# Optimization experiments

Hardware: AMD Instinct MI355X
Metric: run time of the kernel (lower is better)

## Reference

```python
import jax, jax.numpy as jnp
import numpy as np

QLEN, MLEN, B, DM, H, D, NROLL = 512, 512, 8, 1024, 16, 64, 3
KLEN = QLEN + MLEN
SCALE = 1.0 / float(np.sqrt(D))
EPS = 1e-5


def setup_inputs() -> dict:
    key = jax.random.key(0)
    ks = jax.random.split(key, 5)
    h = jax.random.normal(ks[0], (QLEN, B, DM), jnp.float32)
    mems = jax.random.normal(ks[1], (MLEN, B, DM), jnp.float32)
    Wq = jax.random.normal(ks[2], (H * D, DM), jnp.float32) * 0.02
    Wkv = jax.random.normal(ks[3], (2 * H * D, DM), jnp.float32) * 0.02
    Wo = jax.random.normal(ks[4], (DM, H * D), jnp.float32) * 0.02
    ln_gamma = jnp.ones((DM,), jnp.float32)
    ln_beta = jnp.zeros((DM,), jnp.float32)
    # Transformer-XL causal mask over [mems ; h]: query i may attend keys j <= i + MLEN
    attn_mask = jnp.triu(jnp.ones((QLEN, KLEN), dtype=bool), k=1 + MLEN)
    return dict(h=h, mems=mems, Wq=Wq, Wkv=Wkv, Wo=Wo,
                ln_gamma=ln_gamma, ln_beta=ln_beta, attn_mask=attn_mask)


def _dpfp(x):
    # concat(relu(x), relu(-x)) then multiplicative roll expansion (n_roll copies)
    x = jnp.concatenate([jax.nn.relu(x), jax.nn.relu(-x)], axis=-1)  # [..., 2D]
    return jnp.concatenate([x * jnp.roll(x, i, axis=-1) for i in range(1, NROLL + 1)],
                           axis=-1)  # [..., 2*D*NROLL]


def reference(h, mems, Wq, Wkv, Wo, ln_gamma, ln_beta, attn_mask):
    qlen, bsz = h.shape[0], h.shape[1]
    c = jnp.concatenate([mems, h], axis=0)                      # [klen, B, DM]
    klen = c.shape[0]
    q = (h @ Wq.T).reshape(qlen, bsz, H, D)                     # [i, b, n, d]
    k, v = jnp.split(c @ Wkv.T, 2, axis=-1)
    k = k.reshape(klen, bsz, H, D)
    v = v.reshape(klen, bsz, H, D)
    qf = _dpfp(q)                                               # [i, b, n, 2*D*NROLL]
    kf = _dpfp(k)
    score = jnp.einsum('ibnd,jbnd->ijbn', qf, kf) * SCALE        # [i, j, b, n]
    score = jnp.where(attn_mask[:, :, None, None], 0.0, score)
    denom = jnp.sum(score, axis=1, keepdims=True) + EPS
    prob = score / denom
    attn_vec = jnp.einsum('ijbn,jbnd->ibnd', prob, v).reshape(qlen, bsz, H * D)
    attn_out = attn_vec @ Wo.T
    # post-LN residual (pre_lnorm=False)
    x = h + attn_out
    mu = jnp.mean(x, axis=-1, keepdims=True)
    var = jnp.var(x, axis=-1, keepdims=True)
    return (x - mu) / jnp.sqrt(var + EPS) * ln_gamma + ln_beta
```

## Files before the change

### kernel.cpp

```cpp
#include <hip/hip_runtime.h>

#define QLEN 512
#define MLEN 512
#define KLEN 1024
#define BB   8
#define DMODEL 1024
#define NH   16
#define HD   64
#define NF   384
#define ATT_SCALE 0.125f
#define EPSV 1e-5f

typedef float v4f __attribute__((ext_vector_type(4)));
typedef float f32x16 __attribute__((ext_vector_type(16)));
typedef short bf16x8 __attribute__((ext_vector_type(8)));
typedef long lx2 __attribute__((ext_vector_type(2)));
typedef unsigned int u32x4 __attribute__((ext_vector_type(4)));
typedef unsigned int u32x2 __attribute__((ext_vector_type(2)));
typedef unsigned short u16x8 __attribute__((ext_vector_type(8)));

__device__ __forceinline__ unsigned short f2bf(float f) {
    unsigned int x = __builtin_bit_cast(unsigned int, f);
    x += 0x7fffu + ((x >> 16) & 1u);
    return (unsigned short)(x >> 16);
}

__device__ __forceinline__ void gll16(const void* g, void* l) {
    __builtin_amdgcn_global_load_lds(
        (const __attribute__((address_space(1))) unsigned int*)g,
        (__attribute__((address_space(3))) unsigned int*)l, 16, 0, 0);
}


__global__ __launch_bounds__(256)
void cvt_bf16_kernel(const float* __restrict__ src, unsigned short* __restrict__ dst)
{
    int i = (blockIdx.x * 256 + threadIdx.x) * 4;
    v4f v = *(const v4f*)(src + i);
    unsigned int p0, p1;
    asm("v_cvt_pk_bf16_f32 %0, %1, %2" : "=v"(p0) : "v"(v[0]), "v"(v[1]));
    asm("v_cvt_pk_bf16_f32 %0, %1, %2" : "=v"(p1) : "v"(v[2]), "v"(v[3]));
    uint2 u; u.x = p0; u.y = p1;
    *(uint2*)(dst + i) = u;
}

__global__ __launch_bounds__(256)
void cvt_fp8_kernel(const float* __restrict__ h, const float* __restrict__ mems,
                    const float* __restrict__ Wkv, const float* __restrict__ Wq,
                    unsigned char* __restrict__ c8, unsigned char* __restrict__ wkv8,
                    unsigned char* __restrict__ wq8)
{
    int tid = blockIdx.x * 256 + threadIdx.x;
    const float* src; unsigned char* dstrow; float scale; int row, k0;
    if (tid < 1048576) {
        int base = tid * 8; row = base >> 10; k0 = base & 1023;
        src = (row < 4096) ? (mems + (size_t)row * 1024)
                           : (h + (size_t)(row - 4096) * 1024);
        dstrow = c8 + (size_t)row * 1024; scale = 1.f;
    } else if (tid < 1310720) {
        int t2 = tid - 1048576; int base = t2 * 8; row = base >> 10; k0 = base & 1023;
        src = Wkv + (size_t)row * 1024; dstrow = wkv8 + (size_t)row * 1024; scale = 32.f;
    } else {
        int t2 = tid - 1310720; int base = t2 * 8; row = base >> 10; k0 = base & 1023;
        src = Wq + (size_t)row * 1024; dstrow = wq8 + (size_t)row * 1024; scale = 32.f;
    }
    v4f a = *(const v4f*)(src + k0);
    v4f b = *(const v4f*)(src + k0 + 4);
    int v0 = __builtin_amdgcn_cvt_pk_fp8_f32(a[0]*scale, a[1]*scale, 0, false);
    v0     = __builtin_amdgcn_cvt_pk_fp8_f32(a[2]*scale, a[3]*scale, v0, true);
    int v1 = __builtin_amdgcn_cvt_pk_fp8_f32(b[0]*scale, b[1]*scale, 0, false);
    v1     = __builtin_amdgcn_cvt_pk_fp8_f32(b[2]*scale, b[3]*scale, v1, true);
    int kk = (k0 & 127) >> 5;
    int lg = (k0 & 31) >> 3;
    uint2 st; st.x = (unsigned int)v0; st.y = (unsigned int)v1;
    *(uint2*)(dstrow + (k0 & ~127) + (lg * 2 + (kk >> 1)) * 16 + (kk & 1) * 8) = st;
}

__global__ __launch_bounds__(256)
void mmfp8_kernel(const unsigned char* __restrict__ A8,
                  const unsigned char* __restrict__ B8,
                  unsigned short* __restrict__ outK,
                  unsigned short* __restrict__ outV)
{
    __shared__ unsigned char As[2][128 * 128];
    __shared__ unsigned char Bs[2][128 * 128];

    const int t  = threadIdx.x;
    const int w  = t >> 6;
    const int l  = t & 63;
    const int lj = l & 15;
    const int lg = l >> 4;
    const int m0 = blockIdx.x * 128;
    const int n0 = blockIdx.y * 128;
    const int wr = w >> 1, wc = w & 1;

    const int lrow8 = l >> 3;
    const int gsw   = (l & 7) ^ lrow8;

    v4f acc[4][4] = {};

    auto STAGE = [&](int s, int buf) {
        #pragma unroll
        for (int u = 0; u < 4; ++u) {
            int i  = w * 4 + u;
            int so = (i * 8 + lrow8) * 1024 + s * 128 + gsw * 16;
            gll16(A8 + (size_t)m0 * 1024 + so, (char*)As[buf] + i * 1024);
            gll16(B8 + (size_t)n0 * 1024 + so, (char*)Bs[buf] + i * 1024);
        }
    };

    STAGE(0, 0);
    STAGE(1, 1);
    asm volatile("s_waitcnt vmcnt(8)" ::: "memory");
    __builtin_amdgcn_s_barrier();

    for (int s = 0; s < 8; ++s) {
        const int cur = s & 1;

        lx2 a2[4][2], b2[4][2];
        #pragma unroll
        for (int m = 0; m < 4; ++m) {
            int row = wr * 64 + m * 16 + lj;
            #pragma unroll
            for (int gp = 0; gp < 2; ++gp) {
                int gr = lg * 2 + gp;
                a2[m][gp] = *(const lx2*)(As[cur] + row * 128 + ((gr ^ (row & 7)) * 16));
            }
        }
        #pragma unroll
        for (int nn = 0; nn < 4; ++nn) {
            int row = wc * 64 + nn * 16 + lj;
            #pragma unroll
            for (int gp = 0; gp < 2; ++gp) {
                int gr = lg * 2 + gp;
                b2[nn][gp] = *(const lx2*)(Bs[cur] + row * 128 + ((gr ^ (row & 7)) * 16));
            }
        }
        __builtin_amdgcn_s_setprio(1);
        #pragma unroll
        for (int kk = 0; kk < 4; ++kk) {
            #pragma unroll
            for (int m = 0; m < 4; ++m)
                #pragma unroll
                for (int nn = 0; nn < 4; ++nn)
                    acc[m][nn] = __builtin_amdgcn_mfma_f32_16x16x32_fp8_fp8(
                                     a2[m][kk >> 1][kk & 1], b2[nn][kk >> 1][kk & 1],
                                     acc[m][nn], 0, 0, 0);
        }
        __builtin_amdgcn_s_setprio(0);

        if (s == 7) break;
        __builtin_amdgcn_s_barrier();
        if (s < 6) {
            STAGE(s + 2, cur);
            asm volatile("s_waitcnt vmcnt(8)" ::: "memory");
        } else {
            asm volatile("s_waitcnt vmcnt(0)" ::: "memory");
        }
        __builtin_amdgcn_s_barrier();
    }

    #pragma unroll
    for (int m = 0; m < 4; ++m) {
        #pragma unroll
        for (int rr = 0; rr < 4; ++rr) {
            int row = m0 + wr * 64 + m * 16 + 4 * lg + rr;
            #pragma unroll
            for (int nn = 0; nn < 4; ++nn) {
                int col = n0 + wc * 64 + nn * 16 + lj;
                float v = acc[m][nn][rr] * 0.03125f;
                if (n0 < 1024) outK[(size_t)row * 1024 + col] = f2bf(v);
                else           outV[(size_t)row * 1024 + (col - 1024)] = f2bf(v);
            }
        }
    }
}

__global__ __launch_bounds__(256)
void mm128_kernel(const unsigned short* __restrict__ Abf,
                  const unsigned short* __restrict__ Bbf,
                  const float* __restrict__ hres,
                  float* __restrict__ xo)
{
    __shared__ unsigned short As[128 * 64];
    __shared__ unsigned short Bs[128 * 64];

    const int t  = threadIdx.x;
    const int w  = t >> 6;
    const int l  = t & 63;
    const int lj = l & 15;
    const int lg = l >> 4;
    const int m0 = blockIdx.x * 128;
    const int n0 = blockIdx.y * 128;
    const int wr = w >> 1, wc = w & 1;
    const int rsub = l >> 3;
    const int csw  = ((l & 7) ^ rsub) * 16;

    v4f acc[4][4] = {};

    for (int s = 0; s < 16; ++s) {
        const int k0b = s * 128;
        __syncthreads();
        #pragma unroll
        for (int u = 0; u < 4; ++u) {
            int ra = w * 32 + u * 8;
            gll16((const char*)Abf + (size_t)(m0 + ra + rsub) * 2048 + k0b + csw,
                  (char*)As + ra * 128);
            gll16((const char*)Bbf + (size_t)(n0 + ra + rsub) * 2048 + k0b + csw,
                  (char*)Bs + ra * 128);
        }
        __syncthreads();
        #pragma unroll
        for (int ks = 0; ks < 2; ++ks) {
            bf16x8 af[4], bfr[4];
            #pragma unroll
            for (int m = 0; m < 4; ++m) {
                int row = wr * 64 + m * 16 + lj;
                int c = ks * 4 + lg;
                af[m] = *(const bf16x8*)((const char*)As + row * 128 +
                                         ((c ^ (row & 7)) * 16));
            }
            #pragma unroll
            for (int nn = 0; nn < 4; ++nn) {
                int row = wc * 64 + nn * 16 + lj;
                int c = ks * 4 + lg;
                bfr[nn] = *(const bf16x8*)((const char*)Bs + row * 128 +
                                           ((c ^ (row & 7)) * 16));
            }
            #pragma unroll
            for (int m = 0; m < 4; ++m)
                #pragma unroll
                for (int nn = 0; nn < 4; ++nn)
                    acc[m][nn] = __builtin_amdgcn_mfma_f32_16x16x32_bf16(
                                     af[m], bfr[nn], acc[m][nn], 0, 0, 0);
        }
    }

    #pragma unroll
    for (int m = 0; m < 4; ++m) {
        #pragma unroll
        for (int rr = 0; rr < 4; ++rr) {
            int row = m0 + wr * 64 + m * 16 + 4 * lg + rr;
            #pragma unroll
            for (int nn = 0; nn < 4; ++nn) {
                int col = n0 + wc * 64 + nn * 16 + lj;
                xo[(size_t)row * 1024 + col] =
                    acc[m][nn][rr] + hres[(size_t)row * 1024 + col];
            }
        }
    }
}

__device__ __forceinline__ float gld(const unsigned short* gr, int idx) {
    return __builtin_bit_cast(float, ((unsigned int)gr[idx]) << 16);
}

template<int FBASE>
__device__ __forceinline__ void dpfp_half8(const unsigned short* __restrict__ gr,
                                           unsigned char* __restrict__ drow)
{
    #pragma unroll
    for (int c = 0; c < 12; ++c) {
        unsigned int w4[4];
        #pragma unroll
        for (int q4 = 0; q4 < 4; ++q4) {
            float p[4];
            #pragma unroll
            for (int e = 0; e < 4; ++e) {
                const int f  = FBASE + c * 16 + q4 * 4 + e;
                const int r  = (f >> 7) + 1;
                const int tt = f & 127;
                const int uu = (tt - r) & 127;
                p[e] = gld(gr, tt) * gld(gr, uu);
            }
            int v = __builtin_amdgcn_cvt_pk_fp8_f32(p[0], p[1], 0, false);
            v     = __builtin_amdgcn_cvt_pk_fp8_f32(p[2], p[3], v, true);
            w4[q4] = (unsigned int)v;
        }
        u32x4 st = {w4[0], w4[1], w4[2], w4[3]};
        *(u32x4*)(drow + c * 1024) = st;
    }
}

__global__ __launch_bounds__(256)
void dpfp_kernel(const unsigned short* __restrict__ qraw,
                 const unsigned short* __restrict__ kraw,
                 unsigned char* __restrict__ qf, unsigned char* __restrict__ kf)
{
    __shared__ unsigned short G[128 * 138];

    const int t   = threadIdx.x;
    const int blk = blockIdx.x;

    const unsigned short* src; unsigned char* dst; int b, hh, seq0;
    if (blk < 512) {
        int bh = blk >> 2, ig = blk & 3;
        b = bh >> 4; hh = bh & 15; seq0 = ig * 128;
        src = qraw; dst = qf + (size_t)bh * 196608;
    } else {
        int blk2 = blk - 512;
        int bh = blk2 >> 3, jg = blk2 & 7;
        b = bh >> 4; hh = bh & 15; seq0 = jg * 128;
        src = kraw; dst = kf + (size_t)bh * 393216;
    }

    #pragma unroll
    for (int p = 0; p < 4; ++p) {
        int u   = p * 256 + t;
        int row = u >> 3;
        int c0  = (u & 7) * 8;
        u32x4 x = *(const u32x4*)(src + ((size_t)(seq0 + row) * 8 + b) * 1024 +
                                  hh * 64 + c0);
        char* gbase = (char*)G + row * 276 + c0 * 2;
        #pragma unroll
        for (int k = 0; k < 4; ++k) {
            unsigned int xk = x[k];
            float x0 = __builtin_bit_cast(float, xk << 16);
            float x1 = __builtin_bit_cast(float, xk & 0xffff0000u);
            float a0 = fmaxf(x0, 0.f), a1 = fmaxf(x1, 0.f);
            float b0 = fmaxf(-x0, 0.f), b1 = fmaxf(-x1, 0.f);
            unsigned int lo, hig;
            asm("v_cvt_pk_bf16_f32 %0, %1, %2" : "=v"(lo) : "v"(a0), "v"(a1));
            asm("v_cvt_pk_bf16_f32 %0, %1, %2" : "=v"(hig) : "v"(b0), "v"(b1));
            *(unsigned int*)(gbase + k * 4)       = lo;
            *(unsigned int*)(gbase + 128 + k * 4) = hig;
        }
    }
    __syncthreads();

    const int w    = t >> 6;
    const int l    = t & 63;
    const int rowc = (w >> 1) * 64 + l;
    const int hs   = w & 1;
    const unsigned short* gr = G + rowc * 138;
    const int seq = seq0 + rowc;
    unsigned char* drow = dst + (size_t)(seq >> 6) * 24576 + (seq & 63) * 16 +
                          hs * 12288;
    if (hs == 0) dpfp_half8<0>(gr, drow);
    else         dpfp_half8<192>(gr, drow);
}

__global__ __launch_bounds__(256)
void vtrans_kernel(const unsigned short* __restrict__ vraw,
                   unsigned short* __restrict__ vt)
{
    __shared__ unsigned short S[256][72];
    const int t  = threadIdx.x;
    const int jc = blockIdx.x, hh = blockIdx.y, b = blockIdx.z;
    const unsigned short* src = vraw + (size_t)((jc * 256 + t) * 8 + b) * 1024 + hh * 64;
    #pragma unroll
    for (int c = 0; c < 8; ++c)
        *(u32x4*)&S[t][c * 8] = *(const u32x4*)(src + c * 8);
    __syncthreads();
    const int d = t >> 2, qq = t & 3;
    unsigned short* dst = vt + ((size_t)(b * NH + hh) * HD + d) * KLEN + jc * 256 + qq * 64;
    #pragma unroll
    for (int c8 = 0; c8 < 8; ++c8) {
        u16x8 o;
        #pragma unroll
        for (int e = 0; e < 8; ++e) o[e] = S[qq * 64 + c8 * 8 + e][d];
        *(u16x8*)(dst + c8 * 8) = o;
    }
}

__global__ __launch_bounds__(256, 2)
void attn_mfma_kernel(const unsigned char* __restrict__ qf,
                      const unsigned char* __restrict__ kf,
                      const unsigned short* __restrict__ vt,
                      unsigned short* __restrict__ avec)
{
    __shared__ unsigned char Ks[64 * 384];
    __shared__ unsigned short Vs[64 * 64];
    __shared__ float Ds[4][32];

    const int t  = threadIdx.x;
    const int w  = t >> 6;
    const int l  = t & 63;
    const int li = l & 31;
    const int hi = l >> 5;

    const int bid = blockIdx.x;
    const int it  = (bid >> 3) & 3;
    const int P   = ((bid >> 5) << 3) + (bid & 7);
    const int n   = P & 15;
    const int b   = P >> 4;

    const unsigned char* qpan = qf + (size_t)P * 196608;
    const unsigned char* kpan = kf + (size_t)P * 393216;
    const char* vpan = (const char*)(vt + (size_t)P * HD * KLEN);

    int voff[2];
    #pragma unroll
    for (int uu = 0; uu < 2; ++uu) {
        int s  = (w * 2 + uu) * 64 + l;
        int d  = s >> 3;
        int cl = s & 7;
        int cg = cl ^ (d & 7);
        voff[uu] = d * (KLEN * 2) + cg * 16;
    }

    long qfr[24];
    {
        const unsigned char* qb = qpan + (size_t)(it * 2 + (w >> 1)) * 24576 +
                                  ((w & 1) * 32 + li) * 16 + hi * 8;
        #pragma unroll
        for (int ks = 0; ks < 24; ++ks)
            qfr[ks] = *(const long*)(qb + ks * 1024);
    }

    f32x16 num[2] = {};
    float den_acc = 0.f;

    const int ig         = it * 128 + w * 32 + li;
    const int my_jt_end  = 2 * it + 8 + (w >> 1);
    const int jt_blk_end = 2 * it + 9;

    for (int jt = 0; jt <= jt_blk_end; ++jt) {
        __syncthreads();
        const unsigned char* ktile = kpan + (size_t)jt * 24576;
        #pragma unroll
        for (int u = 0; u < 6; ++u)
            gll16(ktile + (w * 6 + u) * 1024 + l * 16, Ks + (w * 6 + u) * 1024);
        const char* vtile = vpan + jt * 128;
        #pragma unroll
        for (int uu = 0; uu < 2; ++uu)
            gll16(vtile + voff[uu], (char*)Vs + (w * 2 + uu) * 1024);
        __syncthreads();

        if (jt > my_jt_end) continue;

        f32x16 sacc0 = {};
        f32x16 sacc1 = {};
        __builtin_amdgcn_s_setprio(1);
        #pragma unroll
        for (int ks = 0; ks < 24; ++ks) {
            long k0 = *(const long*)(Ks + ks * 1024 + li * 16 + hi * 8);
            long k1 = *(const long*)(Ks + ks * 1024 + (32 + li) * 16 + hi * 8);
            sacc0 = __builtin_amdgcn_mfma_f32_32x32x16_fp8_fp8(k0, qfr[ks], sacc0, 0, 0, 0);
            sacc1 = __builtin_amdgcn_mfma_f32_32x32x16_fp8_fp8(k1, qfr[ks], sacc1, 0, 0, 0);
        }
        __builtin_amdgcn_s_setprio(0);

        if (jt == my_jt_end) {
            const int joff = jt * 64 - MLEN + 4 * hi;
            #pragma unroll
            for (int reg = 0; reg < 16; ++reg) {
                int jr = (reg & 3) + 8 * (reg >> 2);
                if (joff + jr > ig)      sacc0[reg] = 0.f;
                if (joff + 32 + jr > ig) sacc1[reg] = 0.f;
            }
        }
        {
            float dpart = 0.f;
            #pragma unroll
            for (int reg = 0; reg < 16; ++reg) dpart += sacc0[reg] + sacc1[reg];
            den_acc += dpart + __shfl_xor(dpart, 32);
        }

        #pragma unroll
        for (int jf = 0; jf < 2; ++jf) {
            const f32x16 sc = jf ? sacc1 : sacc0;
            unsigned int c01, c23, c45, c67, c89, cab, ccd, cef;
            asm("v_cvt_pk_bf16_f32 %0, %1, %2" : "=v"(c01) : "v"(sc[0]),  "v"(sc[1]));
            asm("v_cvt_pk_bf16_f32 %0, %1, %2" : "=v"(c23) : "v"(sc[2]),  "v"(sc[3]));
            asm("v_cvt_pk_bf16_f32 %0, %1, %2" : "=v"(c45) : "v"(sc[4]),  "v"(sc[5]));
            asm("v_cvt_pk_bf16_f32 %0, %1, %2" : "=v"(c67) : "v"(sc[6]),  "v"(sc[7]));
            asm("v_cvt_pk_bf16_f32 %0, %1, %2" : "=v"(c89) : "v"(sc[8]),  "v"(sc[9]));
            asm("v_cvt_pk_bf16_f32 %0, %1, %2" : "=v"(cab) : "v"(sc[10]), "v"(sc[11]));
            asm("v_cvt_pk_bf16_f32 %0, %1, %2" : "=v"(ccd) : "v"(sc[12]), "v"(sc[13]));
            asm("v_cvt_pk_bf16_f32 %0, %1, %2" : "=v"(cef) : "v"(sc[14]), "v"(sc[15]));
            u32x2 r0 = __builtin_amdgcn_permlane32_swap(c01, c45, false, false);
            u32x2 r1 = __builtin_amdgcn_permlane32_swap(c23, c67, false, false);
            u32x2 r2 = __builtin_amdgcn_permlane32_swap(c89, ccd, false, false);
            u32x2 r3 = __builtin_amdgcn_permlane32_swap(cab, cef, false, false);
            u32x4 pw0 = {r0.x, r1.x, r0.y, r1.y};
            u32x4 pw1 = {r2.x, r3.x, r2.y, r3.y};
            bf16x8 pa0 = __builtin_bit_cast(bf16x8, pw0);
            bf16x8 pa1 = __builtin_bit_cast(bf16x8, pw1);
            __builtin_amdgcn_s_setprio(1);
            #pragma unroll
            for (int dd = 0; dd < 2; ++dd) {
                int d = dd * 32 + li;
                {
                    int cs = (jf * 4 + hi) ^ (d & 7);
                    bf16x8 vb = *(const bf16x8*)((const char*)Vs + d * 128 + cs * 16);
                    num[dd] = __builtin_amdgcn_mfma_f32_32x32x16_bf16(pa0, vb, num[dd], 0, 0, 0);
                }
                {
                    int cs = (jf * 4 + 2 + hi) ^ (d & 7);
                    bf16x8 vb = *(const bf16x8*)((const char*)Vs + d * 128 + cs * 16);
                    num[dd] = __builtin_amdgcn_mfma_f32_32x32x16_bf16(pa1, vb, num[dd], 0, 0, 0);
                }
            }
            __builtin_amdgcn_s_setprio(0);
        }
    }

    if (l < 32) Ds[w][l] = den_acc;
    #pragma unroll
    for (int reg = 0; reg < 16; ++reg) {
        int i_loc = (reg & 3) + 8 * (reg >> 2) + 4 * hi;
        float dv = Ds[w][i_loc];
        float minv = ATT_SCALE / (dv * ATT_SCALE + EPSV);
        int ig2 = it * 128 + w * 32 + i_loc;
        unsigned short* orow = avec + ((size_t)ig2 * BB + b) * DMODEL + n * HD;
        orow[li]      = f2bf(num[0][reg] * minv);
        orow[32 + li] = f2bf(num[1][reg] * minv);
    }
}

__global__ __launch_bounds__(256)
void ln_kernel(const float* __restrict__ x, const float* __restrict__ gamma,
               const float* __restrict__ beta, float* __restrict__ out)
{
    const int row = blockIdx.x;
    const int t = threadIdx.x;
    const float* xr = x + (size_t)row * DMODEL;
    v4f xv = *(const v4f*)(xr + (t << 2));
    float s1 = xv[0] + xv[1] + xv[2] + xv[3];
    float s2 = xv[0]*xv[0] + xv[1]*xv[1] + xv[2]*xv[2] + xv[3]*xv[3];
    #pragma unroll
    for (int off = 32; off > 0; off >>= 1) {
        s1 += __shfl_down(s1, off);
        s2 += __shfl_down(s2, off);
    }
    __shared__ float red[2][4];
    __shared__ float mv[2];
    const int wave = t >> 6;
    if ((t & 63) == 0) { red[0][wave] = s1; red[1][wave] = s2; }
    __syncthreads();
    if (t == 0) {
        float a = red[0][0] + red[0][1] + red[0][2] + red[0][3];
        float q = red[1][0] + red[1][1] + red[1][2] + red[1][3];
        float mu  = a * (1.f / DMODEL);
        float var = q * (1.f / DMODEL) - mu * mu;
        mv[0] = mu;
        mv[1] = rsqrtf(var + EPSV);
    }
    __syncthreads();
    float mu = mv[0], rs = mv[1];
    v4f gv = *(const v4f*)(gamma + (t << 2));
    v4f bv = *(const v4f*)(beta + (t << 2));
    v4f o;
    #pragma unroll
    for (int e = 0; e < 4; ++e) o[e] = (xv[e] - mu) * rs * gv[e] + bv[e];
    *(v4f*)(out + (size_t)row * DMODEL + (t << 2)) = o;
}

extern "C" void kernel_launch(void* const* d_in, const int* in_sizes, int n_in,
                              void* d_out, int out_size, void* d_ws, size_t ws_size,
                              hipStream_t stream)
{
    const float* h     = (const float*)d_in[0];
    const float* mems  = (const float*)d_in[1];
    const float* Wq    = (const float*)d_in[2];
    const float* Wkv   = (const float*)d_in[3];
    const float* Wo    = (const float*)d_in[4];
    const float* gamma = (const float*)d_in[5];
    const float* beta  = (const float*)d_in[6];

    char* ws = (char*)d_ws;
    unsigned char* qf    = (unsigned char*)(ws);
    unsigned char* kf    = (unsigned char*)(ws + 25165824);
    unsigned char* c8    = (unsigned char*)(ws + 75497472);
    unsigned char* wkv8  = (unsigned char*)(ws + 83886080);
    unsigned char* wq8   = (unsigned char*)(ws + 85983232);
    unsigned short* kraw = (unsigned short*)(ws + 150994944);
    unsigned short* vt   = kraw;
    unsigned short* vraw = (unsigned short*)(ws + 167772160);
    unsigned short* qraw = (unsigned short*)(ws + 184549376);
    unsigned short* avec = qraw;
    float* xws = (float*)(ws);

    unsigned short* wob = (unsigned short*)d_out;

    cvt_bf16_kernel<<<1024, 256, 0, stream>>>(Wo, wob);
    cvt_fp8_kernel<<<5632, 256, 0, stream>>>(h, mems, Wkv, Wq, c8, wkv8, wq8);
    mmfp8_kernel<<<dim3(64, 16), 256, 0, stream>>>(c8, wkv8, kraw, vraw);
    mmfp8_kernel<<<dim3(32, 8), 256, 0, stream>>>(c8 + 4194304, wq8, qraw, nullptr);
    dpfp_kernel<<<1536, 256, 0, stream>>>(qraw, kraw, qf, kf);
    vtrans_kernel<<<dim3(4, 16, 8), 256, 0, stream>>>(vraw, vt);
    attn_mfma_kernel<<<512, 256, 0, stream>>>(qf, kf, vt, avec);
    mm128_kernel<<<dim3(32, 8), 256, 0, stream>>>(avec, wob, h, xws);
    ln_kernel<<<4096, 256, 0, stream>>>(xws, gamma, beta, (float*)d_out);
}
```

Baseline: 172.7 us.

## Merge prologue kernels into fewer launches and drop fp8 GEMM double buffering

Folds the Wo bf16 conversion into the fp8 conversion kernel. The KV and Q fp8 GEMMs now run as one launch with a grouped tile ordering. The V transpose moves into the dpfp feature kernel, and vt gets its own workspace region so it no longer aliases kraw. The intent is to cut launch overhead and tail gaps between small kernels. In exchange, the GEMM loses its two-stage LDS double buffering and uses a plain single buffer with two syncthreads per k-step, which exposes load latency but halves LDS use.

```diff
diff --git a/kernel.cpp b/kernel.cpp
--- a/kernel.cpp
+++ b/kernel.cpp
@@ -33,24 +33,24 @@
 
 
 __global__ __launch_bounds__(256)
-void cvt_bf16_kernel(const float* __restrict__ src, unsigned short* __restrict__ dst)
-{
-    int i = (blockIdx.x * 256 + threadIdx.x) * 4;
-    v4f v = *(const v4f*)(src + i);
-    unsigned int p0, p1;
-    asm("v_cvt_pk_bf16_f32 %0, %1, %2" : "=v"(p0) : "v"(v[0]), "v"(v[1]));
-    asm("v_cvt_pk_bf16_f32 %0, %1, %2" : "=v"(p1) : "v"(v[2]), "v"(v[3]));
-    uint2 u; u.x = p0; u.y = p1;
-    *(uint2*)(dst + i) = u;
-}
-
-__global__ __launch_bounds__(256)
-void cvt_fp8_kernel(const float* __restrict__ h, const float* __restrict__ mems,
-                    const float* __restrict__ Wkv, const float* __restrict__ Wq,
-                    unsigned char* __restrict__ c8, unsigned char* __restrict__ wkv8,
-                    unsigned char* __restrict__ wq8)
-{
-    int tid = blockIdx.x * 256 + threadIdx.x;
+void cvt_kernel(const float* __restrict__ h, const float* __restrict__ mems,
+                const float* __restrict__ Wkv, const float* __restrict__ Wq,
+                const float* __restrict__ Wo,
+                unsigned char* __restrict__ c8, unsigned char* __restrict__ wkv8,
+                unsigned char* __restrict__ wq8, unsigned short* __restrict__ wob)
+{
+    int blk = blockIdx.x;
+    if (blk >= 5632) {
+        int i = ((blk - 5632) * 256 + threadIdx.x) * 4;
+        v4f v = *(const v4f*)(Wo + i);
+        unsigned int p0, p1;
+        asm("v_cvt_pk_bf16_f32 %0, %1, %2" : "=v"(p0) : "v"(v[0]), "v"(v[1]));
+        asm("v_cvt_pk_bf16_f32 %0, %1, %2" : "=v"(p1) : "v"(v[2]), "v"(v[3]));
+        uint2 u; u.x = p0; u.y = p1;
+        *(uint2*)(wob + i) = u;
+        return;
+    }
+    int tid = blk * 256 + threadIdx.x;
     const float* src; unsigned char* dstrow; float scale; int row, k0;
     if (tid < 1048576) {
         int base = tid * 8; row = base >> 10; k0 = base & 1023;
@@ -77,21 +77,38 @@
 }
 
 __global__ __launch_bounds__(256)
-void mmfp8_kernel(const unsigned char* __restrict__ A8,
-                  const unsigned char* __restrict__ B8,
-                  unsigned short* __restrict__ outK,
-                  unsigned short* __restrict__ outV)
-{
-    __shared__ unsigned char As[2][128 * 128];
-    __shared__ unsigned char Bs[2][128 * 128];
+void mmfp8_kernel(const unsigned char* __restrict__ c8,
+                  const unsigned char* __restrict__ wkv8,
+                  const unsigned char* __restrict__ wq8,
+                  unsigned short* __restrict__ kraw,
+                  unsigned short* __restrict__ vraw,
+                  unsigned short* __restrict__ qraw)
+{
+    __shared__ unsigned char As[128 * 128];
+    __shared__ unsigned char Bs[128 * 128];
+
+    const int bid = blockIdx.x;
+    const unsigned char *A8, *B8;
+    unsigned short *outK, *outV;
+    int m0, n0;
+    if (bid < 1024) {
+        int o = bid & 7, j = bid >> 3;
+        m0 = (o * 8 + (j & 7)) * 128;
+        n0 = (j >> 3) * 128;
+        A8 = c8; B8 = wkv8; outK = kraw; outV = vraw;
+    } else {
+        int d2 = bid - 1024;
+        int o = d2 & 7, j = d2 >> 3;
+        m0 = (o * 4 + (j & 3)) * 128;
+        n0 = (j >> 2) * 128;
+        A8 = c8 + 4194304; B8 = wq8; outK = qraw; outV = nullptr;
+    }
 
     const int t  = threadIdx.x;
     const int w  = t >> 6;
     const int l  = t & 63;
     const int lj = l & 15;
     const int lg = l >> 4;
-    const int m0 = blockIdx.x * 128;
-    const int n0 = blockIdx.y * 128;
     const int wr = w >> 1, wc = w & 1;
 
     const int lrow8 = l >> 3;
@@ -99,23 +116,16 @@
 
     v4f acc[4][4] = {};
 
-    auto STAGE = [&](int s, int buf) {
+    for (int s = 0; s < 8; ++s) {
+        __syncthreads();
         #pragma unroll
         for (int u = 0; u < 4; ++u) {
             int i  = w * 4 + u;
             int so = (i * 8 + lrow8) * 1024 + s * 128 + gsw * 16;
-            gll16(A8 + (size_t)m0 * 1024 + so, (char*)As[buf] + i * 1024);
-            gll16(B8 + (size_t)n0 * 1024 + so, (char*)Bs[buf] + i * 1024);
-        }
-    };
-
-    STAGE(0, 0);
-    STAGE(1, 1);
-    asm volatile("s_waitcnt vmcnt(8)" ::: "memory");
-    __builtin_amdgcn_s_barrier();
-
-    for (int s = 0; s < 8; ++s) {
-        const int cur = s & 1;
+            gll16(A8 + (size_t)m0 * 1024 + so, (char*)As + i * 1024);
+            gll16(B8 + (size_t)n0 * 1024 + so, (char*)Bs + i * 1024);
+        }
+        __syncthreads();
 
         lx2 a2[4][2], b2[4][2];
         #pragma unroll
@@ -124,7 +134,7 @@
             #pragma unroll
             for (int gp = 0; gp < 2; ++gp) {
                 int gr = lg * 2 + gp;
-                a2[m][gp] = *(const lx2*)(As[cur] + row * 128 + ((gr ^ (row & 7)) * 16));
+                a2[m][gp] = *(const lx2*)(As + row * 128 + ((gr ^ (row & 7)) * 16));
             }
         }
         #pragma unroll
@@ -133,7 +143,7 @@
             #pragma unroll
             for (int gp = 0; gp < 2; ++gp) {
                 int gr = lg * 2 + gp;
-                b2[nn][gp] = *(const lx2*)(Bs[cur] + row * 128 + ((gr ^ (row & 7)) * 16));
+                b2[nn][gp] = *(const lx2*)(Bs + row * 128 + ((gr ^ (row & 7)) * 16));
             }
         }
         __builtin_amdgcn_s_setprio(1);
@@ -148,16 +158,6 @@
                                      acc[m][nn], 0, 0, 0);
         }
         __builtin_amdgcn_s_setprio(0);
-
-        if (s == 7) break;
-        __builtin_amdgcn_s_barrier();
-        if (s < 6) {
-            STAGE(s + 2, cur);
-            asm volatile("s_waitcnt vmcnt(8)" ::: "memory");
-        } else {
-            asm volatile("s_waitcnt vmcnt(0)" ::: "memory");
-        }
-        __builtin_amdgcn_s_barrier();
     }
 
     #pragma unroll
@@ -283,15 +283,38 @@
 }
 
 __global__ __launch_bounds__(256)
-void dpfp_kernel(const unsigned short* __restrict__ qraw,
+void feat_kernel(const unsigned short* __restrict__ qraw,
                  const unsigned short* __restrict__ kraw,
-                 unsigned char* __restrict__ qf, unsigned char* __restrict__ kf)
-{
-    __shared__ unsigned short G[128 * 138];
-
+                 const unsigned short* __restrict__ vraw,
+                 unsigned char* __restrict__ qf, unsigned char* __restrict__ kf,
+                 unsigned short* __restrict__ vt)
+{
+    __shared__ __align__(16) char smem[36864];
     const int t   = threadIdx.x;
     const int blk = blockIdx.x;
 
+    if (blk >= 1536) {
+        unsigned short (*S)[72] = (unsigned short(*)[72])smem;
+        int v = blk - 1536;
+        int jc = v & 3, hh = (v >> 2) & 15, b = v >> 6;
+        const unsigned short* src = vraw + (size_t)((jc * 256 + t) * 8 + b) * 1024 + hh * 64;
+        #pragma unroll
+        for (int c = 0; c < 8; ++c)
+            *(u32x4*)&S[t][c * 8] = *(const u32x4*)(src + c * 8);
+        __syncthreads();
+        const int d = t >> 2, qq = t & 3;
+        unsigned short* dst = vt + ((size_t)(b * NH + hh) * HD + d) * KLEN + jc * 256 + qq * 64;
+        #pragma unroll
+        for (int c8 = 0; c8 < 8; ++c8) {
+            u16x8 o;
+            #pragma unroll
+            for (int e = 0; e < 8; ++e) o[e] = S[qq * 64 + c8 * 8 + e][d];
+            *(u16x8*)(dst + c8 * 8) = o;
+        }
+        return;
+    }
+
+    unsigned short* G = (unsigned short*)smem;
     const unsigned short* src; unsigned char* dst; int b, hh, seq0;
     if (blk < 512) {
         int bh = blk >> 2, ig = blk & 3;
@@ -338,29 +361,6 @@
                           hs * 12288;
     if (hs == 0) dpfp_half8<0>(gr, drow);
     else         dpfp_half8<192>(gr, drow);
-}
-
-__global__ __launch_bounds__(256)
-void vtrans_kernel(const unsigned short* __restrict__ vraw,
-                   unsigned short* __restrict__ vt)
-{
-    __shared__ unsigned short S[256][72];
-    const int t  = threadIdx.x;
-    const int jc = blockIdx.x, hh = blockIdx.y, b = blockIdx.z;
-    const unsigned short* src = vraw + (size_t)((jc * 256 + t) * 8 + b) * 1024 + hh * 64;
-    #pragma unroll
-    for (int c = 0; c < 8; ++c)
-        *(u32x4*)&S[t][c * 8] = *(const u32x4*)(src + c * 8);
-    __syncthreads();
-    const int d = t >> 2, qq = t & 3;
-    unsigned short* dst = vt + ((size_t)(b * NH + hh) * HD + d) * KLEN + jc * 256 + qq * 64;
-    #pragma unroll
-    for (int c8 = 0; c8 < 8; ++c8) {
-        u16x8 o;
-        #pragma unroll
-        for (int e = 0; e < 8; ++e) o[e] = S[qq * 64 + c8 * 8 + e][d];
-        *(u16x8*)(dst + c8 * 8) = o;
-    }
 }
 
 __global__ __launch_bounds__(256, 2)
@@ -565,8 +565,8 @@
     unsigned char* c8    = (unsigned char*)(ws + 75497472);
     unsigned char* wkv8  = (unsigned char*)(ws + 83886080);
     unsigned char* wq8   = (unsigned char*)(ws + 85983232);
+    unsigned short* vt   = (unsigned short*)(ws + 92274688);
     unsigned short* kraw = (unsigned short*)(ws + 150994944);
-    unsigned short* vt   = kraw;
     unsigned short* vraw = (unsigned short*)(ws + 167772160);
     unsigned short* qraw = (unsigned short*)(ws + 184549376);
     unsigned short* avec = qraw;
@@ -574,12 +574,9 @@
 
     unsigned short* wob = (unsigned short*)d_out;
 
-    cvt_bf16_kernel<<<1024, 256, 0, stream>>>(Wo, wob);
-    cvt_fp8_kernel<<<5632, 256, 0, stream>>>(h, mems, Wkv, Wq, c8, wkv8, wq8);
-    mmfp8_kernel<<<dim3(64, 16), 256, 0, stream>>>(c8, wkv8, kraw, vraw);
-    mmfp8_kernel<<<dim3(32, 8), 256, 0, stream>>>(c8 + 4194304, wq8, qraw, nullptr);
-    dpfp_kernel<<<1536, 256, 0, stream>>>(qraw, kraw, qf, kf);
-    vtrans_kernel<<<dim3(4, 16, 8), 256, 0, stream>>>(vraw, vt);
+    cvt_kernel<<<6656, 256, 0, stream>>>(h, mems, Wkv, Wq, Wo, c8, wkv8, wq8, wob);
+    mmfp8_kernel<<<1280, 256, 0, stream>>>(c8, wkv8, wq8, kraw, vraw, qraw);
+    feat_kernel<<<2048, 256, 0, stream>>>(qraw, kraw, vraw, qf, kf, vt);
     attn_mfma_kernel<<<512, 256, 0, stream>>>(qf, kf, vt, avec);
     mm128_kernel<<<dim3(32, 8), 256, 0, stream>>>(avec, wob, h, xws);
     ln_kernel<<<4096, 256, 0, stream>>>(xws, gamma, beta, (float*)d_out);
```

Result: faster. 148.4 us, median of 2 (-14.1%).
